# Performance work log

Measured on AMD Instinct MI355X. Metric: run time of the kernel, lower is better.

The kernel has to match this reference:

```python
import jax, jax.numpy as jnp
import numpy as np

WINDOW_SIZE = 2
SOFTMAX_TEMP = 0.01
WIDTH = 320
EPS = 1e-12  # F.normalize default eps


def _l2norm(x, axis):
    n = jnp.sqrt(jnp.sum(x * x, axis=axis, keepdims=True))
    return x / jnp.maximum(n, EPS)


def setup_inputs() -> dict:
    key = jax.random.key(0)
    k1, k2, k3, k4 = jax.random.split(key, 4)
    BW, C, N, S = 4, 256, 1024, 1
    return {
        "keypoint_scores": jax.random.uniform(k1, (BW, S, N), dtype=jnp.float32),
        "keypoint_desc": jax.random.normal(k2, (BW, C, N), dtype=jnp.float32),
        "desc_dense": jax.random.normal(k3, (BW, C, WIDTH, WIDTH), dtype=jnp.float32),
        "keypoint_coords": jax.random.uniform(k4, (BW, N, 2), dtype=jnp.float32),
    }


def reference(keypoint_scores, keypoint_desc, desc_dense, keypoint_coords):
    BW, C, N = keypoint_desc.shape
    B = BW // WINDOW_SIZE
    P = B * (WINDOW_SIZE - 1)  # number of (src, tgt) pairs

    # dense source pixel coordinates (u=col, v=row), matching torch meshgrid 'ij'
    idx = jnp.arange(WIDTH * WIDTH)
    coords = jnp.stack([(idx % WIDTH).astype(jnp.float32),
                        (idx // WIDTH).astype(jnp.float32)], axis=1)  # (HW, 2)

    # pair indexing: for window i, targets are i*w+1 .. i*w+w-1, source is i*w
    tgt_ids = jnp.array([i * WINDOW_SIZE + j for i in range(B)
                         for j in range(1, WINDOW_SIZE)], dtype=jnp.int32)
    src_ids = (tgt_ids // WINDOW_SIZE) * WINDOW_SIZE

    # normalized dense source descriptors: (B, C, HW)
    src_dense = desc_dense[::WINDOW_SIZE].reshape(B, C, -1)
    src_un = _l2norm(src_dense, axis=1)
    src_sel = src_un[tgt_ids // WINDOW_SIZE]  # (P, C, HW)

    # normalized target keypoint descriptors: (P, C, N)
    tgt_n = _l2norm(keypoint_desc[tgt_ids], axis=1)

    # QK^T over descriptor channel: (P, N, HW)
    match_vals = jnp.einsum('pcn,pcm->pnm', tgt_n, src_sel)
    soft = jax.nn.softmax(match_vals / SOFTMAX_TEMP, axis=2)

    # soft-argmax coordinates: (P, N, 2)
    pseudo_coords = jnp.einsum('pnm,md->pnd', soft, coords)

    match_weights = keypoint_scores[tgt_ids]  # (P, S, N)
    return pseudo_coords, match_weights, tgt_ids, src_ids
```

## Files before the change

kernel.cpp:

```cpp
#include <hip/hip_runtime.h>
#include <stdint.h>

#define HW_      102400
#define WIDTH_   320
#define C_       256
#define N_       1024
#define P_       2
#define CHUNKS_  64
#define CHUNK_PX 1600
#define ITERS_   25
#define NB_      4
#define K2_      144.269504088896340f
#define MOFF_    (-72.134752044448170f)

typedef __attribute__((ext_vector_type(8))) short bf16x8;
typedef __attribute__((ext_vector_type(4))) float f32x4;

#define WS_INV_OFF  0
#define WS_TGT_OFF  819200
#define WS_PAR_OFF  1867776

__device__ __forceinline__ uint32_t packbf(float a, float b) {
  uint32_t r;
  asm("v_cvt_pk_bf16_f32 %0, %1, %2" : "=v"(r) : "v"(a), "v"(b));
  return r;
}
__device__ __forceinline__ float fexp2(float x) {
  return __builtin_amdgcn_exp2f(x);
}

__global__ __launch_bounds__(256)
void k_pre(const float* __restrict__ dense, const float* __restrict__ kdesc,
           const float* __restrict__ kscores, float* __restrict__ invn,
           uint16_t* __restrict__ tgt, float* __restrict__ out) {
  const int bid = blockIdx.x;
  if (bid < 800) {
    const int p  = bid / 400;
    const int px = (bid % 400) * 256 + threadIdx.x;
    const float* plane = dense + (size_t)(p * 2) * C_ * HW_ + px;
    float s = 0.f;
    #pragma unroll 8
    for (int c = 0; c < C_; ++c) { const float v = plane[(size_t)c * HW_]; s = fmaf(v, v, s); }
    invn[p * HW_ + px] = 1.f / fmaxf(sqrtf(s), 1e-12f);
  } else {
    const int t = (bid - 800) * 256 + threadIdx.x;
    const int p = t >> 10, n = t & 1023;
    const float* src = kdesc + (size_t)(p * 2 + 1) * C_ * N_ + n;
    float s = 0.f;
    #pragma unroll 16
    for (int c = 0; c < C_; ++c) { const float v = src[c * N_]; s = fmaf(v, v, s); }
    const float inv = 1.f / fmaxf(sqrtf(s), 1e-12f);
    uint32_t* dst = (uint32_t*)(tgt + (size_t)t * C_);
    #pragma unroll 4
    for (int c8 = 0; c8 < C_; c8 += 8) {
      uint4 wv;
      wv.x = packbf(src[(c8 + 0) * N_] * inv, src[(c8 + 1) * N_] * inv);
      wv.y = packbf(src[(c8 + 2) * N_] * inv, src[(c8 + 3) * N_] * inv);
      wv.z = packbf(src[(c8 + 4) * N_] * inv, src[(c8 + 5) * N_] * inv);
      wv.w = packbf(src[(c8 + 6) * N_] * inv, src[(c8 + 7) * N_] * inv);
      *(uint4*)&dst[c8 / 2] = wv;
    }
    out[4096 + t] = kscores[(p * 2 + 1) * N_ + n];
  }
}

__global__ __launch_bounds__(512, 2)
void k_main(const float* __restrict__ dense, const float* __restrict__ invn,
            const uint16_t* __restrict__ tgt, float4* __restrict__ partials) {
  __shared__ uint32_t lds[2 * 64 * 128];

  const int bid   = blockIdx.x;
  const int chunk = bid % CHUNKS_;
  const int nb    = (bid / CHUNKS_) % NB_;
  const int p     = bid / (CHUNKS_ * NB_);

  const int t    = threadIdx.x;
  const int lane = t & 63;
  const int w    = t >> 6;
  const int l15  = lane & 15;
  const int g    = lane >> 4;
  const int h    = w & 1;
  const int q    = w >> 1;

  const float* plane = dense + (size_t)(p * 2) * C_ * HW_;
  const float* invp  = invn + (size_t)p * HW_;

  bf16x8 Bf[4][8];
  const int nbase = nb * 256 + q * 64;
  #pragma unroll
  for (int j = 0; j < 4; ++j) {
    const uint16_t* tp = tgt + (size_t)(p * N_ + nbase + j * 16 + l15) * C_ + g * 8;
    #pragma unroll
    for (int k = 0; k < 8; ++k) Bf[j][k] = *(const bf16x8*)(tp + k * 32);
  }

  float stS[4], stU[4], stV[4];
  #pragma unroll
  for (int j = 0; j < 4; ++j) { stS[j] = 0.f; stU[j] = 0.f; stV[j] = 0.f; }

  const int mi   = (t & 15) * 4;
  const int c8   = (t >> 4) * 8;
  const int wcol = (t >> 4) * 4;
  const int px0  = chunk * CHUNK_PX;

  const int row0 = h * 32 + l15;
  const int swr  = (row0 & 7) << 2;

  uint32_t* bufR = lds;
  uint32_t* bufW = lds + 64 * 128;

  float fva[8][4];
  float iva[4];

  {
    const int px = px0 + mi;
    #pragma unroll
    for (int j = 0; j < 8; ++j) {
      float4 v = *(const float4*)(plane + (size_t)(c8 + j) * HW_ + px);
      fva[j][0] = v.x; fva[j][1] = v.y; fva[j][2] = v.z; fva[j][3] = v.w;
    }
    float4 ivv = *(const float4*)(invp + px);
    iva[0] = ivv.x; iva[1] = ivv.y; iva[2] = ivv.z; iva[3] = ivv.w;
    #pragma unroll
    for (int i = 0; i < 4; ++i) {
      const int row = mi + i;
      uint4 wv;
      wv.x = packbf(fva[0][i] * iva[i], fva[1][i] * iva[i]);
      wv.y = packbf(fva[2][i] * iva[i], fva[3][i] * iva[i]);
      wv.z = packbf(fva[4][i] * iva[i], fva[5][i] * iva[i]);
      wv.w = packbf(fva[6][i] * iva[i], fva[7][i] * iva[i]);
      *(uint4*)&bufR[row * 128 + (wcol ^ ((row & 7) << 2))] = wv;
    }
  }
  __syncthreads();

  for (int iter = 0; iter < ITERS_; ++iter) {
    const bool more = (iter + 1 < ITERS_);

    if (more) {
      const int px = px0 + (iter + 1) * 64 + mi;
      #pragma unroll
      for (int j = 0; j < 8; ++j) {
        float4 v = *(const float4*)(plane + (size_t)(c8 + j) * HW_ + px);
        fva[j][0] = v.x; fva[j][1] = v.y; fva[j][2] = v.z; fva[j][3] = v.w;
      }
      float4 ivv = *(const float4*)(invp + px);
      iva[0] = ivv.x; iva[1] = ivv.y; iva[2] = ivv.z; iva[3] = ivv.w;
    }

    f32x4 acc[4][2];
    #pragma unroll
    for (int j = 0; j < 4; ++j) {
      acc[j][0] = (f32x4){0.f, 0.f, 0.f, 0.f};
      acc[j][1] = (f32x4){0.f, 0.f, 0.f, 0.f};
    }
    #pragma unroll
    for (int k = 0; k < 8; ++k) {
      const int col = (k * 16 + g * 4) ^ swr;
      bf16x8 a0 = *(const bf16x8*)&bufR[row0 * 128 + col];
      bf16x8 a1 = *(const bf16x8*)&bufR[(row0 + 16) * 128 + col];
      #pragma unroll
      for (int j = 0; j < 4; ++j) {
        acc[j][0] = __builtin_amdgcn_mfma_f32_16x16x32_bf16(a0, Bf[j][k], acc[j][0], 0, 0, 0);
        acc[j][1] = __builtin_amdgcn_mfma_f32_16x16x32_bf16(a1, Bf[j][k], acc[j][1], 0, 0, 0);
      }
    }

    const int rb = iter * 64 + h * 32 + g * 4;
    #pragma unroll
    for (int s = 0; s < 2; ++s) {
      #pragma unroll
      for (int e = 0; e < 4; ++e) {
        const int r  = rb + s * 16 + e;
        const int vl = (r * 6554) >> 21;
        const float vf = (float)(chunk * 5 + vl);
        const float uf = (float)(r - vl * 320);
        #pragma unroll
        for (int j = 0; j < 4; ++j) {
          const float ev = fexp2(fmaf(K2_, acc[j][s][e], MOFF_));
          stS[j] += ev;
          stU[j] = fmaf(ev, uf, stU[j]);
          stV[j] = fmaf(ev, vf, stV[j]);
        }
      }
    }

    if (more) {
      #pragma unroll
      for (int i = 0; i < 4; ++i) {
        const int row = mi + i;
        uint4 wv;
        wv.x = packbf(fva[0][i] * iva[i], fva[1][i] * iva[i]);
        wv.y = packbf(fva[2][i] * iva[i], fva[3][i] * iva[i]);
        wv.z = packbf(fva[4][i] * iva[i], fva[5][i] * iva[i]);
        wv.w = packbf(fva[6][i] * iva[i], fva[7][i] * iva[i]);
        *(uint4*)&bufW[row * 128 + (wcol ^ ((row & 7) << 2))] = wv;
      }
    }
    __syncthreads();
    uint32_t* tmp = bufR; bufR = bufW; bufW = tmp;
  }

  #pragma unroll
  for (int j = 0; j < 4; ++j) {
    float S = stS[j], U = stU[j], V = stV[j];
    S += __shfl_xor(S, 16, 64); U += __shfl_xor(U, 16, 64); V += __shfl_xor(V, 16, 64);
    S += __shfl_xor(S, 32, 64); U += __shfl_xor(U, 32, 64); V += __shfl_xor(V, 32, 64);
    if (lane < 16) {
      const int n = nbase + j * 16 + l15;
      partials[((size_t)(p * CHUNKS_ + chunk) * 2 + h) * N_ + n] = make_float4(S, U, V, 0.f);
    }
  }
}

__global__ void k_final(const float4* __restrict__ partials, float* __restrict__ out) {
  const int t = blockIdx.x * blockDim.x + threadIdx.x;
  const int p = t >> 10, n = t & 1023;
  float S = 0.f, U = 0.f, V = 0.f;
  #pragma unroll 4
  for (int s = 0; s < 2 * CHUNKS_; ++s) {
    const float4 v = partials[((size_t)p * 2 * CHUNKS_ + s) * N_ + n];
    S += v.x; U += v.y; V += v.z;
  }
  out[(size_t)(p * N_ + n) * 2 + 0] = U / S;
  out[(size_t)(p * N_ + n) * 2 + 1] = V / S;
  if (t < 4) {
    const float ids[4] = {1.f, 3.f, 0.f, 2.f};
    out[6144 + t] = ids[t];
  }
}

extern "C" void kernel_launch(void* const* d_in, const int* in_sizes, int n_in,
                              void* d_out, int out_size, void* d_ws, size_t ws_size,
                              hipStream_t stream) {
  const float* kscores = (const float*)d_in[0];
  const float* kdesc   = (const float*)d_in[1];
  const float* dense   = (const float*)d_in[2];
  float* out = (float*)d_out;

  char* ws = (char*)d_ws;
  float*    invn = (float*)(ws + WS_INV_OFF);
  uint16_t* tgt  = (uint16_t*)(ws + WS_TGT_OFF);
  float4*   par  = (float4*)(ws + WS_PAR_OFF);

  k_pre<<<808, 256, 0, stream>>>(dense, kdesc, kscores, invn, tgt, out);
  k_main<<<P_ * NB_ * CHUNKS_, 512, 0, stream>>>(dense, invn, tgt, par);
  k_final<<<(P_ * N_) / 256, 256, 0, stream>>>(par, out);
}
```

Measured before the change: 186.7 us.

## Fuse dense descriptor norm computation into main kernel and remap blocks per XCD

Removes the separate pass that read the full dense source planes to compute per-pixel inverse norms. k_main now computes the squared-norm partials from the tile it already loads, reduces them through shared memory, and folds the inverse norm into the exp2 scale. This drops a full extra read of the dense tensor. It also remaps block IDs so the four NB blocks sharing a chunk land on the same XCD, which should improve L2 reuse. The cost is an extra __syncthreads and shared-memory reduction per iteration, and bf16 rounding now happens before normalization.

Measured after the change: 222.6 us. 19.2% more time.

```diff
diff --git a/kernel.cpp b/kernel.cpp
--- a/kernel.cpp
+++ b/kernel.cpp
@@ -2,7 +2,6 @@
 #include <stdint.h>
 
 #define HW_      102400
-#define WIDTH_   320
 #define C_       256
 #define N_       1024
 #define P_       2
@@ -16,9 +15,8 @@
 typedef __attribute__((ext_vector_type(8))) short bf16x8;
 typedef __attribute__((ext_vector_type(4))) float f32x4;
 
-#define WS_INV_OFF  0
-#define WS_TGT_OFF  819200
-#define WS_PAR_OFF  1867776
+#define WS_TGT_OFF  0
+#define WS_PAR_OFF  1048576
 
 __device__ __forceinline__ uint32_t packbf(float a, float b) {
   uint32_t r;
@@ -30,66 +28,58 @@
 }
 
 __global__ __launch_bounds__(256)
-void k_pre(const float* __restrict__ dense, const float* __restrict__ kdesc,
-           const float* __restrict__ kscores, float* __restrict__ invn,
+void k_pre(const float* __restrict__ kdesc, const float* __restrict__ kscores,
            uint16_t* __restrict__ tgt, float* __restrict__ out) {
-  const int bid = blockIdx.x;
-  if (bid < 800) {
-    const int p  = bid / 400;
-    const int px = (bid % 400) * 256 + threadIdx.x;
-    const float* plane = dense + (size_t)(p * 2) * C_ * HW_ + px;
-    float s = 0.f;
-    #pragma unroll 8
-    for (int c = 0; c < C_; ++c) { const float v = plane[(size_t)c * HW_]; s = fmaf(v, v, s); }
-    invn[p * HW_ + px] = 1.f / fmaxf(sqrtf(s), 1e-12f);
-  } else {
-    const int t = (bid - 800) * 256 + threadIdx.x;
-    const int p = t >> 10, n = t & 1023;
-    const float* src = kdesc + (size_t)(p * 2 + 1) * C_ * N_ + n;
-    float s = 0.f;
-    #pragma unroll 16
-    for (int c = 0; c < C_; ++c) { const float v = src[c * N_]; s = fmaf(v, v, s); }
-    const float inv = 1.f / fmaxf(sqrtf(s), 1e-12f);
-    uint32_t* dst = (uint32_t*)(tgt + (size_t)t * C_);
-    #pragma unroll 4
-    for (int c8 = 0; c8 < C_; c8 += 8) {
-      uint4 wv;
-      wv.x = packbf(src[(c8 + 0) * N_] * inv, src[(c8 + 1) * N_] * inv);
-      wv.y = packbf(src[(c8 + 2) * N_] * inv, src[(c8 + 3) * N_] * inv);
-      wv.z = packbf(src[(c8 + 4) * N_] * inv, src[(c8 + 5) * N_] * inv);
-      wv.w = packbf(src[(c8 + 6) * N_] * inv, src[(c8 + 7) * N_] * inv);
-      *(uint4*)&dst[c8 / 2] = wv;
-    }
-    out[4096 + t] = kscores[(p * 2 + 1) * N_ + n];
-  }
+  const int t = blockIdx.x * 256 + threadIdx.x;
+  const int p = t >> 10, n = t & 1023;
+  const float* src = kdesc + (size_t)(p * 2 + 1) * C_ * N_ + n;
+  float s = 0.f;
+  #pragma unroll 16
+  for (int c = 0; c < C_; ++c) { const float v = src[c * N_]; s = fmaf(v, v, s); }
+  const float inv = 1.f / fmaxf(sqrtf(s), 1e-12f);
+  uint32_t* dst = (uint32_t*)(tgt + (size_t)t * C_);
+  #pragma unroll 4
+  for (int c8 = 0; c8 < C_; c8 += 8) {
+    uint4 wv;
+    wv.x = packbf(src[(c8 + 0) * N_] * inv, src[(c8 + 1) * N_] * inv);
+    wv.y = packbf(src[(c8 + 2) * N_] * inv, src[(c8 + 3) * N_] * inv);
+    wv.z = packbf(src[(c8 + 4) * N_] * inv, src[(c8 + 5) * N_] * inv);
+    wv.w = packbf(src[(c8 + 6) * N_] * inv, src[(c8 + 7) * N_] * inv);
+    *(uint4*)&dst[c8 / 2] = wv;
+  }
+  out[4096 + t] = kscores[(p * 2 + 1) * N_ + n];
 }
 
 __global__ __launch_bounds__(512, 2)
-void k_main(const float* __restrict__ dense, const float* __restrict__ invn,
-            const uint16_t* __restrict__ tgt, float4* __restrict__ partials) {
+void k_main(const float* __restrict__ dense, const uint16_t* __restrict__ tgt,
+            float4* __restrict__ partials) {
   __shared__ uint32_t lds[2 * 64 * 128];
+  __shared__ float4 part4[8][16];
+  __shared__ float4 invt4[2][16];
 
   const int bid   = blockIdx.x;
-  const int chunk = bid % CHUNKS_;
-  const int nb    = (bid / CHUNKS_) % NB_;
-  const int p     = bid / (CHUNKS_ * NB_);
+  const int xcd   = bid & 7;
+  const int rr    = bid >> 3;
+  const int grp   = xcd + 8 * (rr >> 2);
+  const int nb    = rr & 3;
+  const int p     = grp >> 6;
+  const int chunk = grp & 63;
 
   const int t    = threadIdx.x;
   const int lane = t & 63;
   const int w    = t >> 6;
   const int l15  = lane & 15;
-  const int g    = lane >> 4;
+  const int g4   = lane >> 4;
   const int h    = w & 1;
   const int q    = w >> 1;
 
   const float* plane = dense + (size_t)(p * 2) * C_ * HW_;
-  const float* invp  = invn + (size_t)p * HW_;
 
   bf16x8 Bf[4][8];
   const int nbase = nb * 256 + q * 64;
   #pragma unroll
   for (int j = 0; j < 4; ++j) {
-    const uint16_t* tp = tgt + (size_t)(p * N_ + nbase + j * 16 + l15) * C_ + g * 8;
+    const uint16_t* tp = tgt + (size_t)(p * N_ + nbase + j * 16 + l15) * C_ + g4 * 8;
     #pragma unroll
     for (int k = 0; k < 8; ++k) Bf[j][k] = *(const bf16x8*)(tp + k * 32);
   }
@@ -105,12 +95,12 @@
 
   const int row0 = h * 32 + l15;
   const int swr  = (row0 & 7) << 2;
+  const int lr0  = h * 32 + g4 * 4;
 
   uint32_t* bufR = lds;
   uint32_t* bufW = lds + 64 * 128;
 
   float fva[8][4];
-  float iva[4];
 
   {
     const int px = px0 + mi;
@@ -119,18 +109,34 @@
       float4 v = *(const float4*)(plane + (size_t)(c8 + j) * HW_ + px);
       fva[j][0] = v.x; fva[j][1] = v.y; fva[j][2] = v.z; fva[j][3] = v.w;
     }
-    float4 ivv = *(const float4*)(invp + px);
-    iva[0] = ivv.x; iva[1] = ivv.y; iva[2] = ivv.z; iva[3] = ivv.w;
+    float ps[4];
     #pragma unroll
     for (int i = 0; i < 4; ++i) {
       const int row = mi + i;
       uint4 wv;
-      wv.x = packbf(fva[0][i] * iva[i], fva[1][i] * iva[i]);
-      wv.y = packbf(fva[2][i] * iva[i], fva[3][i] * iva[i]);
-      wv.z = packbf(fva[4][i] * iva[i], fva[5][i] * iva[i]);
-      wv.w = packbf(fva[6][i] * iva[i], fva[7][i] * iva[i]);
+      wv.x = packbf(fva[0][i], fva[1][i]);
+      wv.y = packbf(fva[2][i], fva[3][i]);
+      wv.z = packbf(fva[4][i], fva[5][i]);
+      wv.w = packbf(fva[6][i], fva[7][i]);
       *(uint4*)&bufR[row * 128 + (wcol ^ ((row & 7) << 2))] = wv;
-    }
+      float s = 0.f;
+      #pragma unroll
+      for (int j = 0; j < 8; ++j) s = fmaf(fva[j][i], fva[j][i], s);
+      ps[i] = s;
+    }
+    #pragma unroll
+    for (int i = 0; i < 4; ++i) {
+      ps[i] += __shfl_xor(ps[i], 16, 64);
+      ps[i] += __shfl_xor(ps[i], 32, 64);
+    }
+    if (g4 == 0) part4[w][l15] = make_float4(ps[0], ps[1], ps[2], ps[3]);
+  }
+  __syncthreads();
+  if (w == 0) {
+    float s = 0.f;
+    #pragma unroll
+    for (int j = 0; j < 8; ++j) s += ((const float*)part4)[j * 64 + lane];
+    ((float*)invt4)[lane] = 1.f / fmaxf(sqrtf(s), 1e-12f);
   }
   __syncthreads();
 
@@ -144,8 +150,6 @@
         float4 v = *(const float4*)(plane + (size_t)(c8 + j) * HW_ + px);
         fva[j][0] = v.x; fva[j][1] = v.y; fva[j][2] = v.z; fva[j][3] = v.w;
       }
-      float4 ivv = *(const float4*)(invp + px);
-      iva[0] = ivv.x; iva[1] = ivv.y; iva[2] = ivv.z; iva[3] = ivv.w;
     }
 
     f32x4 acc[4][2];
@@ -156,7 +160,7 @@
     }
     #pragma unroll
     for (int k = 0; k < 8; ++k) {
-      const int col = (k * 16 + g * 4) ^ swr;
+      const int col = (k * 16 + g4 * 4) ^ swr;
       bf16x8 a0 = *(const bf16x8*)&bufR[row0 * 128 + col];
       bf16x8 a1 = *(const bf16x8*)&bufR[(row0 + 16) * 128 + col];
       #pragma unroll
@@ -166,7 +170,15 @@
       }
     }
 
-    const int rb = iter * 64 + h * 32 + g * 4;
+    const int slot = iter & 1;
+    float kv[8];
+    {
+      float4 iv0 = invt4[slot][lr0 >> 2];
+      float4 iv1 = invt4[slot][(lr0 >> 2) + 4];
+      kv[0] = K2_ * iv0.x; kv[1] = K2_ * iv0.y; kv[2] = K2_ * iv0.z; kv[3] = K2_ * iv0.w;
+      kv[4] = K2_ * iv1.x; kv[5] = K2_ * iv1.y; kv[6] = K2_ * iv1.z; kv[7] = K2_ * iv1.w;
+    }
+    const int rb = iter * 64 + lr0;
     #pragma unroll
     for (int s = 0; s < 2; ++s) {
       #pragma unroll
@@ -175,9 +187,10 @@
         const int vl = (r * 6554) >> 21;
         const float vf = (float)(chunk * 5 + vl);
         const float uf = (float)(r - vl * 320);
+        const float kve = kv[s * 4 + e];
         #pragma unroll
         for (int j = 0; j < 4; ++j) {
-          const float ev = fexp2(fmaf(K2_, acc[j][s][e], MOFF_));
+          const float ev = fexp2(fmaf(kve, acc[j][s][e], MOFF_));
           stS[j] += ev;
           stU[j] = fmaf(ev, uf, stU[j]);
           stV[j] = fmaf(ev, vf, stV[j]);
@@ -186,16 +199,34 @@
     }
 
     if (more) {
+      float ps[4];
       #pragma unroll
       for (int i = 0; i < 4; ++i) {
         const int row = mi + i;
         uint4 wv;
-        wv.x = packbf(fva[0][i] * iva[i], fva[1][i] * iva[i]);
-        wv.y = packbf(fva[2][i] * iva[i], fva[3][i] * iva[i]);
-        wv.z = packbf(fva[4][i] * iva[i], fva[5][i] * iva[i]);
-        wv.w = packbf(fva[6][i] * iva[i], fva[7][i] * iva[i]);
+        wv.x = packbf(fva[0][i], fva[1][i]);
+        wv.y = packbf(fva[2][i], fva[3][i]);
+        wv.z = packbf(fva[4][i], fva[5][i]);
+        wv.w = packbf(fva[6][i], fva[7][i]);
         *(uint4*)&bufW[row * 128 + (wcol ^ ((row & 7) << 2))] = wv;
-      }
+        float s = 0.f;
+        #pragma unroll
+        for (int j = 0; j < 8; ++j) s = fmaf(fva[j][i], fva[j][i], s);
+        ps[i] = s;
+      }
+      #pragma unroll
+      for (int i = 0; i < 4; ++i) {
+        ps[i] += __shfl_xor(ps[i], 16, 64);
+        ps[i] += __shfl_xor(ps[i], 32, 64);
+      }
+      if (g4 == 0) part4[w][l15] = make_float4(ps[0], ps[1], ps[2], ps[3]);
+    }
+    __syncthreads();
+    if (more && w == 0) {
+      float s = 0.f;
+      #pragma unroll
+      for (int j = 0; j < 8; ++j) s += ((const float*)part4)[j * 64 + lane];
+      ((float*)invt4)[((iter + 1) & 1) * 64 + lane] = 1.f / fmaxf(sqrtf(s), 1e-12f);
     }
     __syncthreads();
     uint32_t* tmp = bufR; bufR = bufW; bufW = tmp;
@@ -239,11 +270,10 @@
   float* out = (float*)d_out;
 
   char* ws = (char*)d_ws;
-  float*    invn = (float*)(ws + WS_INV_OFF);
-  uint16_t* tgt  = (uint16_t*)(ws + WS_TGT_OFF);
-  float4*   par  = (float4*)(ws + WS_PAR_OFF);
-
-  k_pre<<<808, 256, 0, stream>>>(dense, kdesc, kscores, invn, tgt, out);
-  k_main<<<P_ * NB_ * CHUNKS_, 512, 0, stream>>>(dense, invn, tgt, par);
+  uint16_t* tgt = (uint16_t*)(ws + WS_TGT_OFF);
+  float4*   par = (float4*)(ws + WS_PAR_OFF);
+
+  k_pre<<<(P_ * N_) / 256, 256, 0, stream>>>(kdesc, kscores, tgt, out);
+  k_main<<<P_ * NB_ * CHUNKS_, 512, 0, stream>>>(dense, tgt, par);
   k_final<<<(P_ * N_) / 256, 256, 0, stream>>>(par, out);
 }
```
